# Optimization experiments

Hardware: AMD Instinct MI355X
Metric: run time of the kernel (lower is better)

## Reference

```python
import jax, jax.numpy as jnp
import numpy as np

BLOCKSIZE = 128
KEEPER = 128


def setup_inputs() -> dict:
    key = jax.random.key(0)
    ks = jax.random.split(key, 8)
    S, H = 2048, 4096
    n_nonout = H - KEEPER          # 3968
    nb = n_nonout // BLOCKSIZE     # 31 low-precision blocks
    return {
        "x": jax.random.normal(ks[0], (1, S, H), dtype=jnp.float32),
        "weight": jax.random.normal(ks[1], (H, H), dtype=jnp.float32),   # [out, in]
        "scales": jax.random.uniform(ks[2], (H, n_nonout), dtype=jnp.float32),
        "keep_scales": jax.random.uniform(ks[3], (H, 1), dtype=jnp.float32),
        "inp_scales_lo": jax.random.uniform(ks[4], (S, nb), dtype=jnp.float32),
        "inp_scales_hi": jax.random.uniform(ks[5], (S, 1), dtype=jnp.float32),
        "inp_base_lo": jax.random.uniform(ks[6], (S, nb), dtype=jnp.float32),
        "inp_base_hi": jax.random.uniform(ks[7], (S, 1), dtype=jnp.float32),
    }


def reference(x, weight, scales, keep_scales, inp_scales_lo, inp_scales_hi,
              inp_base_lo, inp_base_hi):
    # Faithful vectorization of QLinearLayer._forward (channel_group == 0, bias None).
    bs, S, H = x.shape
    xs = x[0]                      # [S, H]  (bs == 1 assert in original)
    W = weight.T                   # [H, O]
    n_nonout = H - KEEPER
    nb = n_nonout // BLOCKSIZE
    O = W.shape[1]

    # Per-block weight scales: scales[:, i1] for each block start i1 -> [nb, O]
    w_blk_scales = scales[:, 0:n_nonout:BLOCKSIZE].T              # [nb, O]

    # Blockwise outer-product scaling fused into the operands:
    # y[s,o] = sum_n sc_lo[s,n] * ws[n,o] * (x_block_n @ W_block_n)[s,o]
    x_lo = xs[:, :n_nonout].reshape(S, nb, BLOCKSIZE) * inp_scales_lo[:, :, None]
    W_lo = W[:n_nonout, :].reshape(nb, BLOCKSIZE, O) * w_blk_scales[:, None, :]
    y = x_lo.reshape(S, n_nonout) @ W_lo.reshape(n_nonout, O)     # [S, O]

    # int8 keeper channels (high-precision path)
    hi_scales = inp_scales_hi @ keep_scales.T                      # [S, O]
    y_hi = xs[:, n_nonout:] @ W[n_nonout:, :]                      # [S, O]
    y = y + y_hi * hi_scales

    return y.reshape(bs, S, O)
```

## Files before the change

kernel.cpp:

```cpp
#include <hip/hip_runtime.h>

#define S_DIM 2048
#define K_DIM 4096
#define O_DIM 4096
#define NNON  3968
#define NB    31

#define XBLK 8192
#define WBLK 16384

typedef __bf16 bf16x8 __attribute__((ext_vector_type(8)));
typedef float  f32x4  __attribute__((ext_vector_type(4)));

__device__ __forceinline__ unsigned short f2bf(float f) {
    union { float f; unsigned u; } v; v.f = f;
    unsigned r = v.u + 0x7FFFu + ((v.u >> 16) & 1u);
    return (unsigned short)(r >> 16);
}

__global__ __launch_bounds__(256) void prepass(const float* __restrict__ x,
                                               const float* __restrict__ sc_lo,
                                               const float* __restrict__ sc_hi,
                                               const float* __restrict__ w,
                                               const float* __restrict__ scales,
                                               const float* __restrict__ keep,
                                               unsigned short* __restrict__ A,
                                               unsigned short* __restrict__ B)
{
    const int b = blockIdx.x;
    if (b < XBLK) {
        int idx = b * 256 + threadIdx.x;
        int s = idx >> 10;
        int k = (idx & 1023) << 2;
        float4 v = ((const float4*)x)[idx];
        float sc = (k < NNON) ? sc_lo[s * NB + (k >> 7)] : sc_hi[s];
        ushort4 o;
        o.x = f2bf(v.x * sc); o.y = f2bf(v.y * sc);
        o.z = f2bf(v.z * sc); o.w = f2bf(v.w * sc);
        ((ushort4*)A)[idx] = o;
    } else {
        int idx = (b - XBLK) * 256 + threadIdx.x;
        int o = idx >> 10;
        int k = (idx & 1023) << 2;
        float4 v = ((const float4*)w)[idx];
        float sc = (k < NNON) ? scales[(size_t)o * NNON + ((k >> 7) << 7)] : keep[o];
        ushort4 r;
        r.x = f2bf(v.x * sc); r.y = f2bf(v.y * sc);
        r.z = f2bf(v.z * sc); r.w = f2bf(v.w * sc);
        ((ushort4*)B)[idx] = r;
    }
}

#define BM 128
#define BN 256
#define BK 64
#define NTILES (K_DIM / BK)
#define NIT (NTILES / 2)

#define GPTR(p) ((__attribute__((address_space(1))) unsigned int*)(p))
#define LPTR(p) ((__attribute__((address_space(3))) unsigned int*)(p))

__device__ __forceinline__ void vm_wait4() { asm volatile("s_waitcnt vmcnt(4)" ::: "memory"); }
__device__ __forceinline__ void vm_wait0() { asm volatile("s_waitcnt vmcnt(0)" ::: "memory"); }
__device__ __forceinline__ void lgkm0()    { asm volatile("s_waitcnt lgkmcnt(0)" ::: "memory"); }
__device__ __forceinline__ void wg_barrier() {
    asm volatile("" ::: "memory");
    __builtin_amdgcn_s_barrier();
    asm volatile("" ::: "memory");
}

__global__ __launch_bounds__(512, 2) void gemm_bt(const unsigned short* __restrict__ A,
                                                  const unsigned short* __restrict__ B,
                                                  float* __restrict__ C)
{
    __shared__ __align__(16) unsigned short As[2][BM * BK];
    __shared__ __align__(16) unsigned short Bs[2][BN * BK];

    const int tid  = threadIdx.x;
    const int wave = tid >> 6;
    const int lane = tid & 63;
    const int quad = lane >> 4;
    const int l16  = lane & 15;

    const int wg = blockIdx.x;
    const int sw = (wg & 7) * 32 + (wg >> 3);
    const int bm = (sw >> 4) * BM;
    const int bn = (sw & 15) * BN;

    const int wn = wave * 32;

    const int r8 = lane >> 3;
    const int q8 = lane & 7;
    const unsigned short* Ag = A + (size_t)(bm + wave * 8 + r8) * K_DIM + ((q8 ^ r8) << 3);
    const unsigned short* Bg = B + (size_t)(bn + wave * 8 + r8) * K_DIM + ((q8 ^ r8) << 3);

    f32x4 acc[8][2];
    #pragma unroll
    for (int ii = 0; ii < 8; ++ii)
        #pragma unroll
        for (int j = 0; j < 2; ++j)
            acc[ii][j] = (f32x4){0.f, 0.f, 0.f, 0.f};

    auto stageA = [&](int buf, int t) {
        unsigned short* dst = &As[buf][(wave * 8) * BK];
        const unsigned short* src = Ag + t * BK;
        #pragma unroll
        for (int s = 0; s < 2; ++s)
            __builtin_amdgcn_global_load_lds(GPTR(src + (size_t)(s * 64) * K_DIM),
                                             LPTR(dst + s * 64 * BK), 16, 0, 0);
    };
    auto stageB = [&](int buf, int t, int h) {
        unsigned short* dst = &Bs[buf][(h * 128 + wave * 8) * BK];
        const unsigned short* src = Bg + (size_t)(h * 128) * K_DIM + t * BK;
        #pragma unroll
        for (int s = 0; s < 2; ++s)
            __builtin_amdgcn_global_load_lds(GPTR(src + (size_t)(s * 64) * K_DIM),
                                             LPTR(dst + s * 64 * BK), 16, 0, 0);
    };

    stageB(0, 0, 0); stageB(0, 0, 1); stageA(0, 0);
    stageB(1, 1, 0); stageB(1, 1, 1);
    vm_wait4();
    wg_barrier();

    const int co0 = ((quad)     ^ (l16 & 7)) << 3;
    const int co1 = ((4 + quad) ^ (l16 & 7)) << 3;

    #pragma unroll 1
    for (int it = 0; it < NIT; ++it) {
        const bool more = (it < NIT - 1);
        const int O  = 2 * it + 1;
        const int E2 = 2 * it + 2;
        const int O2 = 2 * it + 3;

        bf16x8 alo[2][4], ahi[2][4], bf[2][2];

        #pragma unroll
        for (int ii = 0; ii < 4; ++ii) {
            alo[0][ii] = *(const bf16x8*)&As[0][(ii * 16 + l16) * BK + co0];
            alo[1][ii] = *(const bf16x8*)&As[0][(ii * 16 + l16) * BK + co1];
        }
        #pragma unroll
        for (int j = 0; j < 2; ++j) {
            bf[0][j] = *(const bf16x8*)&Bs[0][(wn + j * 16 + l16) * BK + co0];
            bf[1][j] = *(const bf16x8*)&Bs[0][(wn + j * 16 + l16) * BK + co1];
        }
        stageA(1, O);
        wg_barrier(); lgkm0();
        __builtin_amdgcn_s_setprio(1);
        #pragma unroll
        for (int ks = 0; ks < 2; ++ks)
            #pragma unroll
            for (int ii = 0; ii < 4; ++ii)
                #pragma unroll
                for (int j = 0; j < 2; ++j)
                    acc[ii][j] = __builtin_amdgcn_mfma_f32_16x16x32_bf16(alo[ks][ii], bf[ks][j],
                                                                         acc[ii][j], 0, 0, 0);
        __builtin_amdgcn_s_setprio(0);
        wg_barrier();

        #pragma unroll
        for (int ii = 0; ii < 4; ++ii) {
            ahi[0][ii] = *(const bf16x8*)&As[0][((ii + 4) * 16 + l16) * BK + co0];
            ahi[1][ii] = *(const bf16x8*)&As[0][((ii + 4) * 16 + l16) * BK + co1];
        }
        if (more) { stageB(0, E2, 0); stageB(0, E2, 1); }
        wg_barrier(); lgkm0();
        __builtin_amdgcn_s_setprio(1);
        #pragma unroll
        for (int ks = 0; ks < 2; ++ks)
            #pragma unroll
            for (int ii = 0; ii < 4; ++ii)
                #pragma unroll
                for (int j = 0; j < 2; ++j)
                    acc[ii + 4][j] = __builtin_amdgcn_mfma_f32_16x16x32_bf16(ahi[ks][ii], bf[ks][j],
                                                                             acc[ii + 4][j], 0, 0, 0);
        __builtin_amdgcn_s_setprio(0);
        if (more) vm_wait4(); else vm_wait0();
        wg_barrier();

        #pragma unroll
        for (int ii = 0; ii < 4; ++ii) {
            alo[0][ii] = *(const bf16x8*)&As[1][(ii * 16 + l16) * BK + co0];
            alo[1][ii] = *(const bf16x8*)&As[1][(ii * 16 + l16) * BK + co1];
        }
        #pragma unroll
        for (int j = 0; j < 2; ++j) {
            bf[0][j] = *(const bf16x8*)&Bs[1][(wn + j * 16 + l16) * BK + co0];
            bf[1][j] = *(const bf16x8*)&Bs[1][(wn + j * 16 + l16) * BK + co1];
        }
        if (more) stageA(0, E2);
        wg_barrier(); lgkm0();
        __builtin_amdgcn_s_setprio(1);
        #pragma unroll
        for (int ks = 0; ks < 2; ++ks)
            #pragma unroll
            for (int ii = 0; ii < 4; ++ii)
                #pragma unroll
                for (int j = 0; j < 2; ++j)
                    acc[ii][j] = __builtin_amdgcn_mfma_f32_16x16x32_bf16(alo[ks][ii], bf[ks][j],
                                                                         acc[ii][j], 0, 0, 0);
        __builtin_amdgcn_s_setprio(0);
        wg_barrier();

        #pragma unroll
        for (int ii = 0; ii < 4; ++ii) {
            ahi[0][ii] = *(const bf16x8*)&As[1][((ii + 4) * 16 + l16) * BK + co0];
            ahi[1][ii] = *(const bf16x8*)&As[1][((ii + 4) * 16 + l16) * BK + co1];
        }
        if (more) { stageB(1, O2, 0); stageB(1, O2, 1); }
        wg_barrier(); lgkm0();
        __builtin_amdgcn_s_setprio(1);
        #pragma unroll
        for (int ks = 0; ks < 2; ++ks)
            #pragma unroll
            for (int ii = 0; ii < 4; ++ii)
                #pragma unroll
                for (int j = 0; j < 2; ++j)
                    acc[ii + 4][j] = __builtin_amdgcn_mfma_f32_16x16x32_bf16(ahi[ks][ii], bf[ks][j],
                                                                             acc[ii + 4][j], 0, 0, 0);
        __builtin_amdgcn_s_setprio(0);
        if (more) vm_wait4();
        wg_barrier();
    }

    #pragma unroll
    for (int ii = 0; ii < 8; ++ii)
        #pragma unroll
        for (int j = 0; j < 2; ++j) {
            const int col = bn + wn + j * 16 + l16;
            #pragma unroll
            for (int r = 0; r < 4; ++r) {
                const int row = bm + ii * 16 + quad * 4 + r;
                C[(size_t)row * O_DIM + col] = acc[ii][j][r];
            }
        }
}

extern "C" void kernel_launch(void* const* d_in, const int* in_sizes, int n_in,
                              void* d_out, int out_size, void* d_ws, size_t ws_size,
                              hipStream_t stream) {
    const float* x      = (const float*)d_in[0];
    const float* weight = (const float*)d_in[1];
    const float* scales = (const float*)d_in[2];
    const float* keep   = (const float*)d_in[3];
    const float* sc_lo  = (const float*)d_in[4];
    const float* sc_hi  = (const float*)d_in[5];

    unsigned short* A = (unsigned short*)d_ws;
    unsigned short* B = A + (size_t)S_DIM * K_DIM;

    prepass<<<XBLK + WBLK, 256, 0, stream>>>(x, sc_lo, sc_hi, weight, scales, keep, A, B);

    dim3 grid(256);
    gemm_bt<<<grid, 512, 0, stream>>>(A, B, (float*)d_out);
}
```

Before: 257.6 us.

## Split K across wave pairs with 64-wide N tiles and LDS reduction

Each wave now covers 64 output columns over half of each K-chunk, instead of 32 columns over the full chunk. A pair of waves shares an N slice and splits the K halves, then the partial sums are combined through LDS at the end. This cuts the B-fragment LDS reads per MFMA, because each A fragment now feeds four MFMAs instead of two. The cost is doubled accumulator registers (128 floats per lane), which may hurt occupancy under launch_bounds(512,2), plus an extra LDS reduction and barriers in the epilogue.

```diff
diff --git a/kernel.cpp b/kernel.cpp
--- a/kernel.cpp
+++ b/kernel.cpp
@@ -87,18 +87,20 @@
     const int bm = (sw >> 4) * BM;
     const int bn = (sw & 15) * BN;
 
-    const int wn = wave * 32;
+    const int np = wave >> 1;
+    const int kh = wave & 1;
+    const int wn = np * 64;
 
     const int r8 = lane >> 3;
     const int q8 = lane & 7;
     const unsigned short* Ag = A + (size_t)(bm + wave * 8 + r8) * K_DIM + ((q8 ^ r8) << 3);
     const unsigned short* Bg = B + (size_t)(bn + wave * 8 + r8) * K_DIM + ((q8 ^ r8) << 3);
 
-    f32x4 acc[8][2];
+    f32x4 acc[8][4];
     #pragma unroll
     for (int ii = 0; ii < 8; ++ii)
         #pragma unroll
-        for (int j = 0; j < 2; ++j)
+        for (int j = 0; j < 4; ++j)
             acc[ii][j] = (f32x4){0.f, 0.f, 0.f, 0.f};
 
     auto stageA = [&](int buf, int t) {
@@ -123,8 +125,7 @@
     vm_wait4();
     wg_barrier();
 
-    const int co0 = ((quad)     ^ (l16 & 7)) << 3;
-    const int co1 = ((4 + quad) ^ (l16 & 7)) << 3;
+    const int co = (((kh << 2) + quad) ^ (l16 & 7)) << 3;
 
     #pragma unroll 1
     for (int it = 0; it < NIT; ++it) {
@@ -133,108 +134,119 @@
         const int E2 = 2 * it + 2;
         const int O2 = 2 * it + 3;
 
-        bf16x8 alo[2][4], ahi[2][4], bf[2][2];
-
-        #pragma unroll
-        for (int ii = 0; ii < 4; ++ii) {
-            alo[0][ii] = *(const bf16x8*)&As[0][(ii * 16 + l16) * BK + co0];
-            alo[1][ii] = *(const bf16x8*)&As[0][(ii * 16 + l16) * BK + co1];
+        bf16x8 af[8], bf[4];
+
+        #pragma unroll
+        for (int ii = 0; ii < 4; ++ii)
+            af[ii] = *(const bf16x8*)&As[0][(ii * 16 + l16) * BK + co];
+        #pragma unroll
+        for (int j = 0; j < 4; ++j)
+            bf[j] = *(const bf16x8*)&Bs[0][(wn + j * 16 + l16) * BK + co];
+        stageA(1, O);
+        wg_barrier(); lgkm0();
+        __builtin_amdgcn_s_setprio(1);
+        #pragma unroll
+        for (int ii = 0; ii < 4; ++ii)
+            #pragma unroll
+            for (int j = 0; j < 4; ++j)
+                acc[ii][j] = __builtin_amdgcn_mfma_f32_16x16x32_bf16(af[ii], bf[j],
+                                                                     acc[ii][j], 0, 0, 0);
+        __builtin_amdgcn_s_setprio(0);
+        wg_barrier();
+
+        #pragma unroll
+        for (int ii = 4; ii < 8; ++ii)
+            af[ii] = *(const bf16x8*)&As[0][(ii * 16 + l16) * BK + co];
+        if (more) { stageB(0, E2, 0); stageB(0, E2, 1); }
+        wg_barrier(); lgkm0();
+        __builtin_amdgcn_s_setprio(1);
+        #pragma unroll
+        for (int ii = 4; ii < 8; ++ii)
+            #pragma unroll
+            for (int j = 0; j < 4; ++j)
+                acc[ii][j] = __builtin_amdgcn_mfma_f32_16x16x32_bf16(af[ii], bf[j],
+                                                                     acc[ii][j], 0, 0, 0);
+        __builtin_amdgcn_s_setprio(0);
+        if (more) vm_wait4(); else vm_wait0();
+        wg_barrier();
+
+        #pragma unroll
+        for (int ii = 0; ii < 4; ++ii)
+            af[ii] = *(const bf16x8*)&As[1][(ii * 16 + l16) * BK + co];
+        #pragma unroll
+        for (int j = 0; j < 4; ++j)
+            bf[j] = *(const bf16x8*)&Bs[1][(wn + j * 16 + l16) * BK + co];
+        if (more) stageA(0, E2);
+        wg_barrier(); lgkm0();
+        __builtin_amdgcn_s_setprio(1);
+        #pragma unroll
+        for (int ii = 0; ii < 4; ++ii)
+            #pragma unroll
+            for (int j = 0; j < 4; ++j)
+                acc[ii][j] = __builtin_amdgcn_mfma_f32_16x16x32_bf16(af[ii], bf[j],
+                                                                     acc[ii][j], 0, 0, 0);
+        __builtin_amdgcn_s_setprio(0);
+        wg_barrier();
+
+        #pragma unroll
+        for (int ii = 4; ii < 8; ++ii)
+            af[ii] = *(const bf16x8*)&As[1][(ii * 16 + l16) * BK + co];
+        if (more) { stageB(1, O2, 0); stageB(1, O2, 1); }
+        wg_barrier(); lgkm0();
+        __builtin_amdgcn_s_setprio(1);
+        #pragma unroll
+        for (int ii = 4; ii < 8; ++ii)
+            #pragma unroll
+            for (int j = 0; j < 4; ++j)
+                acc[ii][j] = __builtin_amdgcn_mfma_f32_16x16x32_bf16(af[ii], bf[j],
+                                                                     acc[ii][j], 0, 0, 0);
+        __builtin_amdgcn_s_setprio(0);
+        if (more) vm_wait4();
+        wg_barrier();
+    }
+
+    {
+        float* xch = (float*)&Bs[0][0];
+        const int lbase = np * 4096 + lane * 64;
+        #pragma unroll
+        for (int round = 0; round < 2; ++round) {
+            if (kh == 1) {
+                #pragma unroll
+                for (int ii = 0; ii < 8; ++ii)
+                    #pragma unroll
+                    for (int jj = 0; jj < 2; ++jj) {
+                        const int c = ii * 2 + jj;
+                        *(f32x4*)&xch[lbase + ((c ^ l16) << 2)] = acc[ii][round * 2 + jj];
+                    }
+            }
+            wg_barrier();
+            if (kh == 0) {
+                #pragma unroll
+                for (int ii = 0; ii < 8; ++ii)
+                    #pragma unroll
+                    for (int jj = 0; jj < 2; ++jj) {
+                        const int c = ii * 2 + jj;
+                        f32x4 p = *(const f32x4*)&xch[lbase + ((c ^ l16) << 2)];
+                        acc[ii][round * 2 + jj] += p;
+                    }
+            }
+            wg_barrier();
         }
-        #pragma unroll
-        for (int j = 0; j < 2; ++j) {
-            bf[0][j] = *(const bf16x8*)&Bs[0][(wn + j * 16 + l16) * BK + co0];
-            bf[1][j] = *(const bf16x8*)&Bs[0][(wn + j * 16 + l16) * BK + co1];
-        }
-        stageA(1, O);
-        wg_barrier(); lgkm0();
-        __builtin_amdgcn_s_setprio(1);
-        #pragma unroll
-        for (int ks = 0; ks < 2; ++ks)
-            #pragma unroll
-            for (int ii = 0; ii < 4; ++ii)
+    }
+
+    if (kh == 0) {
+        #pragma unroll
+        for (int ii = 0; ii < 8; ++ii)
+            #pragma unroll
+            for (int j = 0; j < 4; ++j) {
+                const int col = bn + wn + j * 16 + l16;
                 #pragma unroll
-                for (int j = 0; j < 2; ++j)
-                    acc[ii][j] = __builtin_amdgcn_mfma_f32_16x16x32_bf16(alo[ks][ii], bf[ks][j],
-                                                                         acc[ii][j], 0, 0, 0);
-        __builtin_amdgcn_s_setprio(0);
-        wg_barrier();
-
-        #pragma unroll
-        for (int ii = 0; ii < 4; ++ii) {
-            ahi[0][ii] = *(const bf16x8*)&As[0][((ii + 4) * 16 + l16) * BK + co0];
-            ahi[1][ii] = *(const bf16x8*)&As[0][((ii + 4) * 16 + l16) * BK + co1];
-        }
-        if (more) { stageB(0, E2, 0); stageB(0, E2, 1); }
-        wg_barrier(); lgkm0();
-        __builtin_amdgcn_s_setprio(1);
-        #pragma unroll
-        for (int ks = 0; ks < 2; ++ks)
-            #pragma unroll
-            for (int ii = 0; ii < 4; ++ii)
-                #pragma unroll
-                for (int j = 0; j < 2; ++j)
-                    acc[ii + 4][j] = __builtin_amdgcn_mfma_f32_16x16x32_bf16(ahi[ks][ii], bf[ks][j],
-                                                                             acc[ii + 4][j], 0, 0, 0);
-        __builtin_amdgcn_s_setprio(0);
-        if (more) vm_wait4(); else vm_wait0();
-        wg_barrier();
-
-        #pragma unroll
-        for (int ii = 0; ii < 4; ++ii) {
-            alo[0][ii] = *(const bf16x8*)&As[1][(ii * 16 + l16) * BK + co0];
-            alo[1][ii] = *(const bf16x8*)&As[1][(ii * 16 + l16) * BK + co1];
-        }
-        #pragma unroll
-        for (int j = 0; j < 2; ++j) {
-            bf[0][j] = *(const bf16x8*)&Bs[1][(wn + j * 16 + l16) * BK + co0];
-            bf[1][j] = *(const bf16x8*)&Bs[1][(wn + j * 16 + l16) * BK + co1];
-        }
-        if (more) stageA(0, E2);
-        wg_barrier(); lgkm0();
-        __builtin_amdgcn_s_setprio(1);
-        #pragma unroll
-        for (int ks = 0; ks < 2; ++ks)
-            #pragma unroll
-            for (int ii = 0; ii < 4; ++ii)
-                #pragma unroll
-                for (int j = 0; j < 2; ++j)
-                    acc[ii][j] = __builtin_amdgcn_mfma_f32_16x16x32_bf16(alo[ks][ii], bf[ks][j],
-                                                                         acc[ii][j], 0, 0, 0);
-        __builtin_amdgcn_s_setprio(0);
-        wg_barrier();
-
-        #pragma unroll
-        for (int ii = 0; ii < 4; ++ii) {
-            ahi[0][ii] = *(const bf16x8*)&As[1][((ii + 4) * 16 + l16) * BK + co0];
-            ahi[1][ii] = *(const bf16x8*)&As[1][((ii + 4) * 16 + l16) * BK + co1];
-        }
-        if (more) { stageB(1, O2, 0); stageB(1, O2, 1); }
-        wg_barrier(); lgkm0();
-        __builtin_amdgcn_s_setprio(1);
-        #pragma unroll
-        for (int ks = 0; ks < 2; ++ks)
-            #pragma unroll
-            for (int ii = 0; ii < 4; ++ii)
-                #pragma unroll
-                for (int j = 0; j < 2; ++j)
-                    acc[ii + 4][j] = __builtin_amdgcn_mfma_f32_16x16x32_bf16(ahi[ks][ii], bf[ks][j],
-                                                                             acc[ii + 4][j], 0, 0, 0);
-        __builtin_amdgcn_s_setprio(0);
-        if (more) vm_wait4();
-        wg_barrier();
-    }
-
-    #pragma unroll
-    for (int ii = 0; ii < 8; ++ii)
-        #pragma unroll
-        for (int j = 0; j < 2; ++j) {
-            const int col = bn + wn + j * 16 + l16;
-            #pragma unroll
-            for (int r = 0; r < 4; ++r) {
-                const int row = bm + ii * 16 + quad * 4 + r;
-                C[(size_t)row * O_DIM + col] = acc[ii][j][r];
+                for (int r = 0; r < 4; ++r) {
+                    const int row = bm + ii * 16 + quad * 4 + r;
+                    C[(size_t)row * O_DIM + col] = acc[ii][j][r];
+                }
             }
-        }
+    }
 }
 
 extern "C" void kernel_launch(void* const* d_in, const int* in_sizes, int n_in,
```

After: 254.1 us. No clear change (-1.4%).

## Use 256x256 tiles with split-K over two slices and atomic accumulation

Applied to the files above, without the earlier changes.

The GEMM tile grows from 128x256 to 256x256 with a 2x4 wave layout, so each wave computes a 128x64 sub-tile. To keep 256 workgroups, K is split into two halves, each handled by a separate workgroup whose partial results are added into the output with float atomics. The output is zeroed with a memset before the kernels run. The larger tile raises operand reuse from LDS and cuts global traffic per FLOP, at the cost of more accumulator registers, a memset pass, atomic write traffic, and run-to-run variation in the order of the two partial sums.

```diff
diff --git a/kernel.cpp b/kernel.cpp
--- a/kernel.cpp
+++ b/kernel.cpp
@@ -51,15 +51,17 @@
     }
 }
 
-#define BM 128
+#define BM 256
 #define BN 256
 #define BK 64
-#define NTILES (K_DIM / BK)
-#define NIT (NTILES / 2)
+#define KSLICE 2048
+#define NTK (KSLICE / BK)
+#define NIT (NTK / 2)
 
 #define GPTR(p) ((__attribute__((address_space(1))) unsigned int*)(p))
 #define LPTR(p) ((__attribute__((address_space(3))) unsigned int*)(p))
 
+__device__ __forceinline__ void vm_wait6() { asm volatile("s_waitcnt vmcnt(6)" ::: "memory"); }
 __device__ __forceinline__ void vm_wait4() { asm volatile("s_waitcnt vmcnt(4)" ::: "memory"); }
 __device__ __forceinline__ void vm_wait0() { asm volatile("s_waitcnt vmcnt(0)" ::: "memory"); }
 __device__ __forceinline__ void lgkm0()    { asm volatile("s_waitcnt lgkmcnt(0)" ::: "memory"); }
@@ -82,35 +84,38 @@
     const int quad = lane >> 4;
     const int l16  = lane & 15;
 
-    const int wg = blockIdx.x;
-    const int sw = (wg & 7) * 32 + (wg >> 3);
-    const int bm = (sw >> 4) * BM;
-    const int bn = (sw & 15) * BN;
-
-    const int wn = wave * 32;
+    const int wg  = blockIdx.x;
+    const int sw  = (wg & 7) * 32 + (wg >> 3);
+    const int bm  = (sw >> 5) * BM;
+    const int bn  = ((sw >> 1) & 15) * BN;
+    const int ksl = sw & 1;
+    const int kbase = ksl * KSLICE;
+
+    const int wm = (wave >> 2) * 128;
+    const int wn = (wave & 3) * 64;
 
     const int r8 = lane >> 3;
     const int q8 = lane & 7;
-    const unsigned short* Ag = A + (size_t)(bm + wave * 8 + r8) * K_DIM + ((q8 ^ r8) << 3);
-    const unsigned short* Bg = B + (size_t)(bn + wave * 8 + r8) * K_DIM + ((q8 ^ r8) << 3);
-
-    f32x4 acc[8][2];
+    const unsigned short* Ag = A + (size_t)(bm + wave * 8 + r8) * K_DIM + kbase + ((q8 ^ r8) << 3);
+    const unsigned short* Bg = B + (size_t)(bn + wave * 8 + r8) * K_DIM + kbase + ((q8 ^ r8) << 3);
+
+    f32x4 acc[8][4];
     #pragma unroll
     for (int ii = 0; ii < 8; ++ii)
         #pragma unroll
-        for (int j = 0; j < 2; ++j)
+        for (int j = 0; j < 4; ++j)
             acc[ii][j] = (f32x4){0.f, 0.f, 0.f, 0.f};
 
-    auto stageA = [&](int buf, int t) {
-        unsigned short* dst = &As[buf][(wave * 8) * BK];
-        const unsigned short* src = Ag + t * BK;
+    auto stageA = [&](int t, int h) {
+        unsigned short* dst = &As[t & 1][(h * 128 + wave * 8) * BK];
+        const unsigned short* src = Ag + (size_t)(h * 128) * K_DIM + t * BK;
         #pragma unroll
         for (int s = 0; s < 2; ++s)
             __builtin_amdgcn_global_load_lds(GPTR(src + (size_t)(s * 64) * K_DIM),
                                              LPTR(dst + s * 64 * BK), 16, 0, 0);
     };
-    auto stageB = [&](int buf, int t, int h) {
-        unsigned short* dst = &Bs[buf][(h * 128 + wave * 8) * BK];
+    auto stageB = [&](int t, int h) {
+        unsigned short* dst = &Bs[t & 1][(h * 128 + wave * 8) * BK];
         const unsigned short* src = Bg + (size_t)(h * 128) * K_DIM + t * BK;
         #pragma unroll
         for (int s = 0; s < 2; ++s)
@@ -118,9 +123,9 @@
                                              LPTR(dst + s * 64 * BK), 16, 0, 0);
     };
 
-    stageB(0, 0, 0); stageB(0, 0, 1); stageA(0, 0);
-    stageB(1, 1, 0); stageB(1, 1, 1);
-    vm_wait4();
+    stageB(0, 0); stageA(0, 0); stageA(0, 1); stageB(0, 1);
+    stageB(1, 0); stageB(1, 1); stageA(1, 0);
+    vm_wait6();
     wg_barrier();
 
     const int co0 = ((quad)     ^ (l16 & 7)) << 3;
@@ -130,50 +135,82 @@
     for (int it = 0; it < NIT; ++it) {
         const bool more = (it < NIT - 1);
         const int O  = 2 * it + 1;
-        const int E2 = 2 * it + 2;
-        const int O2 = 2 * it + 3;
-
-        bf16x8 alo[2][4], ahi[2][4], bf[2][2];
+        const int En = 2 * it + 2;
+        const int On = 2 * it + 3;
+
+        bf16x8 alo[2][4], ahi[2][4], b0[2][2], b1[2][2];
 
         #pragma unroll
         for (int ii = 0; ii < 4; ++ii) {
-            alo[0][ii] = *(const bf16x8*)&As[0][(ii * 16 + l16) * BK + co0];
-            alo[1][ii] = *(const bf16x8*)&As[0][(ii * 16 + l16) * BK + co1];
+            alo[0][ii] = *(const bf16x8*)&As[0][(wm + ii * 16 + l16) * BK + co0];
+            alo[1][ii] = *(const bf16x8*)&As[0][(wm + ii * 16 + l16) * BK + co1];
         }
         #pragma unroll
         for (int j = 0; j < 2; ++j) {
-            bf[0][j] = *(const bf16x8*)&Bs[0][(wn + j * 16 + l16) * BK + co0];
-            bf[1][j] = *(const bf16x8*)&Bs[0][(wn + j * 16 + l16) * BK + co1];
-        }
-        stageA(1, O);
-        wg_barrier(); lgkm0();
-        __builtin_amdgcn_s_setprio(1);
-        #pragma unroll
-        for (int ks = 0; ks < 2; ++ks)
-            #pragma unroll
-            for (int ii = 0; ii < 4; ++ii)
-                #pragma unroll
-                for (int j = 0; j < 2; ++j)
-                    acc[ii][j] = __builtin_amdgcn_mfma_f32_16x16x32_bf16(alo[ks][ii], bf[ks][j],
+            b0[0][j] = *(const bf16x8*)&Bs[0][(wn + j * 16 + l16) * BK + co0];
+            b0[1][j] = *(const bf16x8*)&Bs[0][(wn + j * 16 + l16) * BK + co1];
+        }
+        stageA(O, 1);
+        wg_barrier(); lgkm0();
+        __builtin_amdgcn_s_setprio(1);
+        #pragma unroll
+        for (int ks = 0; ks < 2; ++ks)
+            #pragma unroll
+            for (int ii = 0; ii < 4; ++ii)
+                #pragma unroll
+                for (int j = 0; j < 2; ++j)
+                    acc[ii][j] = __builtin_amdgcn_mfma_f32_16x16x32_bf16(alo[ks][ii], b0[ks][j],
                                                                          acc[ii][j], 0, 0, 0);
         __builtin_amdgcn_s_setprio(0);
         wg_barrier();
 
         #pragma unroll
+        for (int j = 0; j < 2; ++j) {
+            b1[0][j] = *(const bf16x8*)&Bs[0][(wn + 32 + j * 16 + l16) * BK + co0];
+            b1[1][j] = *(const bf16x8*)&Bs[0][(wn + 32 + j * 16 + l16) * BK + co1];
+        }
+        wg_barrier(); lgkm0();
+        __builtin_amdgcn_s_setprio(1);
+        #pragma unroll
+        for (int ks = 0; ks < 2; ++ks)
+            #pragma unroll
+            for (int ii = 0; ii < 4; ++ii)
+                #pragma unroll
+                for (int j = 0; j < 2; ++j)
+                    acc[ii][j + 2] = __builtin_amdgcn_mfma_f32_16x16x32_bf16(alo[ks][ii], b1[ks][j],
+                                                                             acc[ii][j + 2], 0, 0, 0);
+        __builtin_amdgcn_s_setprio(0);
+        wg_barrier();
+
+        #pragma unroll
         for (int ii = 0; ii < 4; ++ii) {
-            ahi[0][ii] = *(const bf16x8*)&As[0][((ii + 4) * 16 + l16) * BK + co0];
-            ahi[1][ii] = *(const bf16x8*)&As[0][((ii + 4) * 16 + l16) * BK + co1];
-        }
-        if (more) { stageB(0, E2, 0); stageB(0, E2, 1); }
-        wg_barrier(); lgkm0();
-        __builtin_amdgcn_s_setprio(1);
-        #pragma unroll
-        for (int ks = 0; ks < 2; ++ks)
-            #pragma unroll
-            for (int ii = 0; ii < 4; ++ii)
-                #pragma unroll
-                for (int j = 0; j < 2; ++j)
-                    acc[ii + 4][j] = __builtin_amdgcn_mfma_f32_16x16x32_bf16(ahi[ks][ii], bf[ks][j],
+            ahi[0][ii] = *(const bf16x8*)&As[0][(wm + 64 + ii * 16 + l16) * BK + co0];
+            ahi[1][ii] = *(const bf16x8*)&As[0][(wm + 64 + ii * 16 + l16) * BK + co1];
+        }
+        if (more) stageB(En, 0);
+        wg_barrier(); lgkm0();
+        __builtin_amdgcn_s_setprio(1);
+        #pragma unroll
+        for (int ks = 0; ks < 2; ++ks)
+            #pragma unroll
+            for (int ii = 0; ii < 4; ++ii)
+                #pragma unroll
+                for (int j = 0; j < 2; ++j)
+                    acc[ii + 4][j + 2] = __builtin_amdgcn_mfma_f32_16x16x32_bf16(ahi[ks][ii], b1[ks][j],
+                                                                                 acc[ii + 4][j + 2], 0, 0, 0);
+        __builtin_amdgcn_s_setprio(0);
+        wg_barrier();
+
+        if (more) stageA(En, 0);
+        wg_barrier();
+        __builtin_amdgcn_s_setprio(1);
+        #pragma unroll
+        for (int ks = 0; ks < 2; ++ks)
+            #pragma unroll
+            for (int ii = 0; ii < 4; ++ii)
+                #pragma unroll
+                for (int j = 0; j < 2; ++j)
+                    acc[ii + 4][j] = __builtin_amdgcn_mfma_f32_16x16x32_bf16(ahi[ks][ii], b0[ks][j],
                                                                              acc[ii + 4][j], 0, 0, 0);
         __builtin_amdgcn_s_setprio(0);
         if (more) vm_wait4(); else vm_wait0();
@@ -181,58 +218,90 @@
 
         #pragma unroll
         for (int ii = 0; ii < 4; ++ii) {
-            alo[0][ii] = *(const bf16x8*)&As[1][(ii * 16 + l16) * BK + co0];
-            alo[1][ii] = *(const bf16x8*)&As[1][(ii * 16 + l16) * BK + co1];
+            alo[0][ii] = *(const bf16x8*)&As[1][(wm + ii * 16 + l16) * BK + co0];
+            alo[1][ii] = *(const bf16x8*)&As[1][(wm + ii * 16 + l16) * BK + co1];
         }
         #pragma unroll
         for (int j = 0; j < 2; ++j) {
-            bf[0][j] = *(const bf16x8*)&Bs[1][(wn + j * 16 + l16) * BK + co0];
-            bf[1][j] = *(const bf16x8*)&Bs[1][(wn + j * 16 + l16) * BK + co1];
-        }
-        if (more) stageA(0, E2);
-        wg_barrier(); lgkm0();
-        __builtin_amdgcn_s_setprio(1);
-        #pragma unroll
-        for (int ks = 0; ks < 2; ++ks)
-            #pragma unroll
-            for (int ii = 0; ii < 4; ++ii)
-                #pragma unroll
-                for (int j = 0; j < 2; ++j)
-                    acc[ii][j] = __builtin_amdgcn_mfma_f32_16x16x32_bf16(alo[ks][ii], bf[ks][j],
+            b0[0][j] = *(const bf16x8*)&Bs[1][(wn + j * 16 + l16) * BK + co0];
+            b0[1][j] = *(const bf16x8*)&Bs[1][(wn + j * 16 + l16) * BK + co1];
+        }
+        if (more) { stageA(En, 1); stageB(En, 1); }
+        wg_barrier(); lgkm0();
+        __builtin_amdgcn_s_setprio(1);
+        #pragma unroll
+        for (int ks = 0; ks < 2; ++ks)
+            #pragma unroll
+            for (int ii = 0; ii < 4; ++ii)
+                #pragma unroll
+                for (int j = 0; j < 2; ++j)
+                    acc[ii][j] = __builtin_amdgcn_mfma_f32_16x16x32_bf16(alo[ks][ii], b0[ks][j],
                                                                          acc[ii][j], 0, 0, 0);
         __builtin_amdgcn_s_setprio(0);
         wg_barrier();
 
         #pragma unroll
+        for (int j = 0; j < 2; ++j) {
+            b1[0][j] = *(const bf16x8*)&Bs[1][(wn + 32 + j * 16 + l16) * BK + co0];
+            b1[1][j] = *(const bf16x8*)&Bs[1][(wn + 32 + j * 16 + l16) * BK + co1];
+        }
+        wg_barrier(); lgkm0();
+        __builtin_amdgcn_s_setprio(1);
+        #pragma unroll
+        for (int ks = 0; ks < 2; ++ks)
+            #pragma unroll
+            for (int ii = 0; ii < 4; ++ii)
+                #pragma unroll
+                for (int j = 0; j < 2; ++j)
+                    acc[ii][j + 2] = __builtin_amdgcn_mfma_f32_16x16x32_bf16(alo[ks][ii], b1[ks][j],
+                                                                             acc[ii][j + 2], 0, 0, 0);
+        __builtin_amdgcn_s_setprio(0);
+        wg_barrier();
+
+        #pragma unroll
         for (int ii = 0; ii < 4; ++ii) {
-            ahi[0][ii] = *(const bf16x8*)&As[1][((ii + 4) * 16 + l16) * BK + co0];
-            ahi[1][ii] = *(const bf16x8*)&As[1][((ii + 4) * 16 + l16) * BK + co1];
-        }
-        if (more) { stageB(1, O2, 0); stageB(1, O2, 1); }
-        wg_barrier(); lgkm0();
-        __builtin_amdgcn_s_setprio(1);
-        #pragma unroll
-        for (int ks = 0; ks < 2; ++ks)
-            #pragma unroll
-            for (int ii = 0; ii < 4; ++ii)
-                #pragma unroll
-                for (int j = 0; j < 2; ++j)
-                    acc[ii + 4][j] = __builtin_amdgcn_mfma_f32_16x16x32_bf16(ahi[ks][ii], bf[ks][j],
+            ahi[0][ii] = *(const bf16x8*)&As[1][(wm + 64 + ii * 16 + l16) * BK + co0];
+            ahi[1][ii] = *(const bf16x8*)&As[1][(wm + 64 + ii * 16 + l16) * BK + co1];
+        }
+        if (more) stageB(On, 0);
+        wg_barrier(); lgkm0();
+        __builtin_amdgcn_s_setprio(1);
+        #pragma unroll
+        for (int ks = 0; ks < 2; ++ks)
+            #pragma unroll
+            for (int ii = 0; ii < 4; ++ii)
+                #pragma unroll
+                for (int j = 0; j < 2; ++j)
+                    acc[ii + 4][j + 2] = __builtin_amdgcn_mfma_f32_16x16x32_bf16(ahi[ks][ii], b1[ks][j],
+                                                                                 acc[ii + 4][j + 2], 0, 0, 0);
+        __builtin_amdgcn_s_setprio(0);
+        wg_barrier();
+
+        if (more) { stageA(On, 0); stageB(On, 1); }
+        wg_barrier();
+        __builtin_amdgcn_s_setprio(1);
+        #pragma unroll
+        for (int ks = 0; ks < 2; ++ks)
+            #pragma unroll
+            for (int ii = 0; ii < 4; ++ii)
+                #pragma unroll
+                for (int j = 0; j < 2; ++j)
+                    acc[ii + 4][j] = __builtin_amdgcn_mfma_f32_16x16x32_bf16(ahi[ks][ii], b0[ks][j],
                                                                              acc[ii + 4][j], 0, 0, 0);
         __builtin_amdgcn_s_setprio(0);
-        if (more) vm_wait4();
+        if (more) vm_wait6();
         wg_barrier();
     }
 
     #pragma unroll
     for (int ii = 0; ii < 8; ++ii)
         #pragma unroll
-        for (int j = 0; j < 2; ++j) {
+        for (int j = 0; j < 4; ++j) {
             const int col = bn + wn + j * 16 + l16;
             #pragma unroll
             for (int r = 0; r < 4; ++r) {
-                const int row = bm + ii * 16 + quad * 4 + r;
-                C[(size_t)row * O_DIM + col] = acc[ii][j][r];
+                const int row = bm + wm + ii * 16 + quad * 4 + r;
+                unsafeAtomicAdd(&C[(size_t)row * O_DIM + col], acc[ii][j][r]);
             }
         }
 }
@@ -250,6 +319,7 @@
     unsigned short* A = (unsigned short*)d_ws;
     unsigned short* B = A + (size_t)S_DIM * K_DIM;
 
+    hipMemsetAsync(d_out, 0, (size_t)S_DIM * O_DIM * sizeof(float), stream);
     prepass<<<XBLK + WBLK, 256, 0, stream>>>(x, sc_lo, sc_hi, weight, scales, keep, A, B);
 
     dim3 grid(256);
```

Result: slower. 290.9 us (+12.9%).
